# Kernel tuning notes

Measured on AMD Instinct MI355X. Metric: run time of the kernel, lower is better.

Reference implementation:

```python
import jax, jax.numpy as jnp
import numpy as np
import math

N = 100000      # num vertices
M = 50000       # num hyperedges
NNZ = 800000    # incidence entries
F_IN = 128
NHID = 128
NCLS = 40
DEPTH = 4
ALPHA = 0.1     # restart_alpha
LAMDA = 0.5


def setup_inputs() -> dict:
    key = jax.random.key(0)
    ks = jax.random.split(key, 8)
    x = jax.random.normal(ks[0], (N, F_IN), jnp.float32)
    vertex = jax.random.randint(ks[1], (NNZ,), 0, N)
    edges = jax.random.randint(ks[2], (NNZ,), 0, M)
    s0 = 1.0 / np.sqrt(F_IN)
    sh = 1.0 / np.sqrt(NHID)
    W0 = jax.random.uniform(ks[3], (F_IN, NHID), jnp.float32, -s0, s0)
    b0 = jax.random.uniform(ks[4], (NHID,), jnp.float32, -s0, s0)
    Ws = jax.random.uniform(ks[5], (DEPTH, NHID, NHID), jnp.float32, -sh, sh)
    Wout = jax.random.uniform(ks[6], (NHID, NCLS), jnp.float32, -sh, sh)
    bout = jax.random.uniform(ks[7], (NCLS,), jnp.float32, -sh, sh)
    return {"x": x, "W0": W0, "b0": b0, "Ws": Ws, "Wout": Wout,
            "bout": bout, "vertex": vertex, "edges": edges}


def reference(x, W0, b0, Ws, Wout, bout, vertex, edges):
    ones = jnp.ones((NNZ, 1), x.dtype)
    cnt_e = jnp.maximum(jax.ops.segment_sum(ones, edges, num_segments=M), 1.0)
    cnt_v = jnp.maximum(jax.ops.segment_sum(ones, vertex, num_segments=N), 1.0)

    x = jax.nn.relu(x @ W0 + b0)
    x0 = x
    for i in range(DEPTH):
        beta = math.log(LAMDA / (i + 1) + 1.0)
        # vertex -> edge mean aggregation
        Xve = x[vertex]                                          # [NNZ, NHID]
        Xe = jax.ops.segment_sum(Xve, edges, num_segments=M) / cnt_e
        # edge -> vertex mean aggregation
        Xev = Xe[edges]                                          # [NNZ, NHID]
        Xv = jax.ops.segment_sum(Xev, vertex, num_segments=N) / cnt_v
        # L2 row-normalize with detached scale (use_norm=True)
        norm = jnp.linalg.norm(Xv, axis=1, keepdims=True)
        scale = jax.lax.stop_gradient(jnp.where(norm > 0, 1.0 / norm, 0.0))
        Xv = Xv * scale
        # alpha/beta residual blend (UniGCNII)
        Xi = (1.0 - ALPHA) * Xv + ALPHA * x0
        x = jax.nn.relu((1.0 - beta) * Xi + beta * (Xi @ Ws[i]))
    return x @ Wout + bout
```

## Files before the change

kernel.cpp:

```cpp
#include <hip/hip_runtime.h>

#define NV 100000
#define NE 50000
#define NNZ_C 800000
#define CAP_E 64
#define CAP_V 48

typedef unsigned int uint32;
typedef unsigned short u16;
typedef u16 u16x8 __attribute__((ext_vector_type(8)));
typedef short short8 __attribute__((ext_vector_type(8)));
typedef float floatx4 __attribute__((ext_vector_type(4)));

__device__ __forceinline__ float bf2f(u16 h) {
  return __uint_as_float(((uint32)h) << 16);
}
__device__ __forceinline__ u16 f2bf(float f) {
  uint32 u = __float_as_uint(f);
  u += 0x7FFF + ((u >> 16) & 1);
  return (u16)(u >> 16);
}


__global__ void zero_cursors(int4* p, int n4) {
  int stride = gridDim.x * blockDim.x;
  for (int i = blockIdx.x * blockDim.x + threadIdx.x; i < n4; i += stride)
    p[i] = make_int4(0, 0, 0, 0);
}

__global__ void fill_kernel(const int* __restrict__ vertex, const int* __restrict__ edges,
                            int* __restrict__ cntE, int* __restrict__ cntV,
                            int* __restrict__ itemsE, int* __restrict__ itemsV) {
  int stride = gridDim.x * blockDim.x;
  for (int k = blockIdx.x * blockDim.x + threadIdx.x; k < NNZ_C; k += stride) {
    int e = edges[k], v = vertex[k];
    int pe = atomicAdd(&cntE[e << 4], 1);
    if (pe < CAP_E) itemsE[e * CAP_E + pe] = v;
    int pv = atomicAdd(&cntV[v << 4], 1);
    if (pv < CAP_V) itemsV[v * CAP_V + pv] = e;
  }
}


__global__ void prep_weights(const float* __restrict__ W0, const float* __restrict__ Ws,
                             u16* __restrict__ WT) {
  int idx = blockIdx.x * blockDim.x + threadIdx.x;
  if (idx >= 5 * 16384) return;
  const float betas[4] = {0.4054651081f, 0.2231435513f, 0.1541506798f, 0.1177830357f};
  int sec = idx >> 14;
  int rc = idx & 16383;
  int n = rc >> 7, k = rc & 127;
  float v;
  if (sec == 0) {
    v = W0[k * 128 + n];
  } else {
    int i = sec - 1;
    float b = betas[i];
    v = b * Ws[i * 16384 + k * 128 + n];
    if (k == n) v += 1.0f - b;
  }
  WT[idx] = f2bf(v);
}

__global__ void convert_x(const float* __restrict__ x, u16* __restrict__ xh) {
  int idx = blockIdx.x * blockDim.x + threadIdx.x;
  const float4* p = (const float4*)(x + (size_t)idx * 8);
  float4 a = p[0], b = p[1];
  u16x8 o;
  o[0] = f2bf(a.x); o[1] = f2bf(a.y); o[2] = f2bf(a.z); o[3] = f2bf(a.w);
  o[4] = f2bf(b.x); o[5] = f2bf(b.y); o[6] = f2bf(b.z); o[7] = f2bf(b.w);
  *(u16x8*)(xh + (size_t)idx * 8) = o;
}


__global__ __launch_bounds__(256) void edge_agg(const u16* __restrict__ Xh,
                                                const int* __restrict__ cntE,
                                                const int* __restrict__ itemsE,
                                                u16* __restrict__ Xeh) {
  int g = threadIdx.x >> 4;
  int lane = threadIdx.x & 15;
  int e = blockIdx.x * 16 + g;
  int cnt = cntE[e << 4];
  int n = min(cnt, CAP_E);
  const int* it = itemsE + e * CAP_E;
  float acc[8] = {0.f, 0.f, 0.f, 0.f, 0.f, 0.f, 0.f, 0.f};
  int j = 0;
  for (; j + 4 <= n; j += 4) {
    int4 vs = *(const int4*)(it + j);
    u16x8 a = *(const u16x8*)(Xh + (size_t)vs.x * 128 + lane * 8);
    u16x8 b = *(const u16x8*)(Xh + (size_t)vs.y * 128 + lane * 8);
    u16x8 c = *(const u16x8*)(Xh + (size_t)vs.z * 128 + lane * 8);
    u16x8 d = *(const u16x8*)(Xh + (size_t)vs.w * 128 + lane * 8);
    #pragma unroll
    for (int q = 0; q < 8; q++)
      acc[q] += (bf2f(a[q]) + bf2f(b[q])) + (bf2f(c[q]) + bf2f(d[q]));
  }
  for (; j < n; j++) {
    int v = it[j];
    u16x8 xv = *(const u16x8*)(Xh + (size_t)v * 128 + lane * 8);
    #pragma unroll
    for (int q = 0; q < 8; q++) acc[q] += bf2f(xv[q]);
  }
  float inv = 1.f / fmaxf((float)cnt, 1.f);
  u16x8 o;
  #pragma unroll
  for (int q = 0; q < 8; q++) o[q] = f2bf(acc[q] * inv);
  *(u16x8*)(Xeh + (size_t)e * 128 + lane * 8) = o;
}

__global__ __launch_bounds__(256) void vertex_agg(const u16* __restrict__ Xeh,
                                                  const int* __restrict__ cntV,
                                                  const int* __restrict__ itemsV,
                                                  const u16* __restrict__ x0h,
                                                  u16* __restrict__ Xih) {
  int g = threadIdx.x >> 4;
  int lane = threadIdx.x & 15;
  int v = blockIdx.x * 16 + g;
  int cnt = cntV[v << 4];
  int n = min(cnt, CAP_V);
  const int* it = itemsV + v * CAP_V;
  float acc[8] = {0.f, 0.f, 0.f, 0.f, 0.f, 0.f, 0.f, 0.f};
  int j = 0;
  for (; j + 4 <= n; j += 4) {
    int4 es = *(const int4*)(it + j);
    u16x8 a = *(const u16x8*)(Xeh + (size_t)es.x * 128 + lane * 8);
    u16x8 b = *(const u16x8*)(Xeh + (size_t)es.y * 128 + lane * 8);
    u16x8 c = *(const u16x8*)(Xeh + (size_t)es.z * 128 + lane * 8);
    u16x8 d = *(const u16x8*)(Xeh + (size_t)es.w * 128 + lane * 8);
    #pragma unroll
    for (int q = 0; q < 8; q++)
      acc[q] += (bf2f(a[q]) + bf2f(b[q])) + (bf2f(c[q]) + bf2f(d[q]));
  }
  for (; j < n; j++) {
    int e = it[j];
    u16x8 xv = *(const u16x8*)(Xeh + (size_t)e * 128 + lane * 8);
    #pragma unroll
    for (int q = 0; q < 8; q++) acc[q] += bf2f(xv[q]);
  }
  float inv = 1.f / fmaxf((float)cnt, 1.f);
  float sq = 0.f;
  #pragma unroll
  for (int q = 0; q < 8; q++) { acc[q] *= inv; sq += acc[q] * acc[q]; }
  sq += __shfl_xor(sq, 1, 64);
  sq += __shfl_xor(sq, 2, 64);
  sq += __shfl_xor(sq, 4, 64);
  sq += __shfl_xor(sq, 8, 64);
  float scale = (sq > 0.f) ? rsqrtf(sq) : 0.f;
  u16x8 x0v = *(const u16x8*)(x0h + (size_t)v * 128 + lane * 8);
  u16x8 o;
  #pragma unroll
  for (int q = 0; q < 8; q++)
    o[q] = f2bf(0.9f * acc[q] * scale + 0.1f * bf2f(x0v[q]));
  *(u16x8*)(Xih + (size_t)v * 128 + lane * 8) = o;
}


__global__ __launch_bounds__(256) void gemm_mfma(const u16* __restrict__ Ah,
                                                 const u16* __restrict__ WT,
                                                 const float* __restrict__ bias,
                                                 u16* __restrict__ Yh,
                                                 u16* __restrict__ Y2h, int nrows) {
  __shared__ u16 As[128 * 136];
  __shared__ u16 Bs[128 * 136];
  int t = threadIdx.x;
  int row0 = blockIdx.x * 128;
  #pragma unroll
  for (int i = 0; i < 8; i++) {
    int idx = t + 256 * i;
    int r = idx >> 4, c8 = idx & 15;
    u16x8 v = {0, 0, 0, 0, 0, 0, 0, 0};
    if (row0 + r < nrows) v = *(const u16x8*)(Ah + (size_t)(row0 + r) * 128 + c8 * 8);
    *(u16x8*)&As[r * 136 + c8 * 8] = v;
    u16x8 wv = *(const u16x8*)(WT + (size_t)r * 128 + c8 * 8);
    *(u16x8*)&Bs[r * 136 + c8 * 8] = wv;
  }
  __syncthreads();

  int w = t >> 6;
  int lane = t & 63;
  int lo16 = lane & 15, hi = lane >> 4;
  floatx4 acc[2][8];
  #pragma unroll
  for (int rt = 0; rt < 2; rt++)
    #pragma unroll
    for (int ct = 0; ct < 8; ct++) acc[rt][ct] = (floatx4){0.f, 0.f, 0.f, 0.f};

  #pragma unroll
  for (int kc = 0; kc < 4; kc++) {
    int koff = kc * 32 + hi * 8;
    short8 a0 = *(const short8*)&As[(w * 32 + lo16) * 136 + koff];
    short8 a1 = *(const short8*)&As[(w * 32 + 16 + lo16) * 136 + koff];
    #pragma unroll
    for (int ct = 0; ct < 8; ct++) {
      short8 b = *(const short8*)&Bs[(ct * 16 + lo16) * 136 + koff];
      acc[0][ct] = __builtin_amdgcn_mfma_f32_16x16x32_bf16(a0, b, acc[0][ct], 0, 0, 0);
      acc[1][ct] = __builtin_amdgcn_mfma_f32_16x16x32_bf16(a1, b, acc[1][ct], 0, 0, 0);
    }
  }
  __syncthreads();

  #pragma unroll
  for (int rt = 0; rt < 2; rt++) {
    #pragma unroll
    for (int ct = 0; ct < 8; ct++) {
      int col = ct * 16 + lo16;
      float bv = bias ? bias[col] : 0.f;
      #pragma unroll
      for (int reg = 0; reg < 4; reg++) {
        int row = w * 32 + rt * 16 + hi * 4 + reg;
        float v = acc[rt][ct][reg] + bv;
        v = fmaxf(v, 0.f);
        As[row * 136 + col] = f2bf(v);
      }
    }
  }
  __syncthreads();
  #pragma unroll
  for (int i = 0; i < 8; i++) {
    int idx = t + 256 * i;
    int r = idx >> 4, c8 = idx & 15;
    if (row0 + r < nrows) {
      u16x8 v = *(const u16x8*)&As[r * 136 + c8 * 8];
      *(u16x8*)(Yh + (size_t)(row0 + r) * 128 + c8 * 8) = v;
      if (Y2h) *(u16x8*)(Y2h + (size_t)(row0 + r) * 128 + c8 * 8) = v;
    }
  }
}


__global__ __launch_bounds__(256) void gemm_out(const u16* __restrict__ Xh,
                                                const float* __restrict__ W,
                                                const float* __restrict__ bias,
                                                float* __restrict__ Y, int nrows) {
  __shared__ float xs[128][36];
  __shared__ float ws[32][44];
  int t = threadIdx.x;
  int tr = t >> 3;
  int tc = t & 7;
  int row0 = blockIdx.x * 128;
  float acc[4][5];
  #pragma unroll
  for (int i = 0; i < 4; i++)
    #pragma unroll
    for (int j = 0; j < 5; j++) acc[i][j] = 0.f;

  for (int k0 = 0; k0 < 128; k0 += 32) {
    #pragma unroll
    for (int i = 0; i < 2; i++) {
      int idx = t + 256 * i;
      int r = idx >> 2, c8 = idx & 3;
      int gr = row0 + r;
      u16x8 v = {0, 0, 0, 0, 0, 0, 0, 0};
      if (gr < nrows) v = *(const u16x8*)(Xh + (size_t)gr * 128 + k0 + c8 * 8);
      #pragma unroll
      for (int q = 0; q < 8; q++) xs[r][c8 * 8 + q] = bf2f(v[q]);
    }
    #pragma unroll
    for (int i = 0; i < 5; i++) {
      int idx = t + 256 * i;
      int r = idx / 40, c = idx % 40;
      ws[r][c] = W[(k0 + r) * 40 + c];
    }
    __syncthreads();
    #pragma unroll
    for (int kk4 = 0; kk4 < 8; kk4++) {
      float4 xv[4];
      #pragma unroll
      for (int i = 0; i < 4; i++) xv[i] = *(const float4*)&xs[tr + 32 * i][kk4 * 4];
      #pragma unroll
      for (int q = 0; q < 4; q++) {
        int kk = kk4 * 4 + q;
        float w[5];
        #pragma unroll
        for (int j = 0; j < 5; j++) w[j] = ws[kk][tc * 5 + j];
        #pragma unroll
        for (int i = 0; i < 4; i++) {
          float xq = ((const float*)&xv[i])[q];
          #pragma unroll
          for (int j = 0; j < 5; j++) acc[i][j] += xq * w[j];
        }
      }
    }
    __syncthreads();
  }
  #pragma unroll
  for (int i = 0; i < 4; i++) {
    int gr = row0 + tr + 32 * i;
    if (gr >= nrows) continue;
    #pragma unroll
    for (int j = 0; j < 5; j++) {
      int c = tc * 5 + j;
      Y[(long)gr * 40 + c] = acc[i][j] + bias[c];
    }
  }
}


extern "C" void kernel_launch(void* const* d_in, const int* in_sizes, int n_in,
                              void* d_out, int out_size, void* d_ws, size_t ws_size,
                              hipStream_t stream) {
  const float* x    = (const float*)d_in[0];
  const float* W0   = (const float*)d_in[1];
  const float* b0   = (const float*)d_in[2];
  const float* Ws   = (const float*)d_in[3];
  const float* Wout = (const float*)d_in[4];
  const float* bout = (const float*)d_in[5];
  const int* vertex = (const int*)d_in[6];
  const int* edges  = (const int*)d_in[7];
  float* out = (float*)d_out;

  char* base = (char*)d_ws;
  size_t o = 0;
  auto alloc = [&](size_t bytes) -> char* {
    char* r = base + o;
    o += (bytes + 255) & ~(size_t)255;
    return r;
  };
  u16* xh     = (u16*)alloc((size_t)NV * 128 * 2);
  u16* x_curh = (u16*)alloc((size_t)NV * 128 * 2);
  u16* x0h    = (u16*)alloc((size_t)NV * 128 * 2);
  u16* Xeh    = (u16*)alloc((size_t)NE * 128 * 2);
  u16* WT     = (u16*)alloc((size_t)5 * 16384 * 2);
  int* cntE   = (int*)alloc((size_t)NE * 16 * 4);
  int* cntV   = (int*)alloc((size_t)NV * 16 * 4);
  int* itemsE = (int*)alloc((size_t)NE * CAP_E * 4);
  int* itemsV = (int*)alloc((size_t)NV * CAP_V * 4);

  int n4 = (NE * 16 + NV * 16) / 4;
  zero_cursors<<<1024, 256, 0, stream>>>((int4*)cntE, n4);
  fill_kernel<<<1024, 256, 0, stream>>>(vertex, edges, cntE, cntV, itemsE, itemsV);
  prep_weights<<<(5 * 16384 + 255) / 256, 256, 0, stream>>>(W0, Ws, WT);
  convert_x<<<(NV * 128 / 8 + 255) / 256, 256, 0, stream>>>(x, xh);

  int gblocks = (NV + 127) / 128;
  gemm_mfma<<<gblocks, 256, 0, stream>>>(xh, WT, b0, x_curh, x0h, NV);

  for (int i = 0; i < 4; i++) {
    edge_agg<<<NE / 16, 256, 0, stream>>>(x_curh, cntE, itemsE, Xeh);
    vertex_agg<<<NV / 16, 256, 0, stream>>>(Xeh, cntV, itemsV, x0h, x_curh);
    gemm_mfma<<<gblocks, 256, 0, stream>>>(x_curh, WT + (size_t)(1 + i) * 16384,
                                           nullptr, x_curh, nullptr, NV);
  }
  gemm_out<<<gblocks, 256, 0, stream>>>(x_curh, Wout, bout, out, NV);
}
```

Measured before the change: 577.1 us.

## Bucket-sort incidence build, fuse vertex aggregation into GEMM, fold x conversion

Incidence-list construction now runs in two passes: a coarse scatter into 128-key buckets packed as (local key, value) words, then a per-bucket expansion that uses shared-memory atomics for the per-key cursors. This is meant to replace the global atomics on padded per-key counters. The vertex aggregation, normalization and residual blend are fused into the layer GEMM, so Xi is built straight into LDS and never round-trips through global memory. The fp32-to-bf16 conversion of x is folded into the first GEMM's load. The cost is that the fused GEMM runs only 782 blocks, each serially gathering 128 rows, which lowers the parallelism of the gather phase.

Result: slower. 701.7 us (+21.6%).

```diff
diff --git a/kernel.cpp b/kernel.cpp
--- a/kernel.cpp
+++ b/kernel.cpp
@@ -5,6 +5,10 @@
 #define NNZ_C 800000
 #define CAP_E 64
 #define CAP_V 48
+#define NB_E 391
+#define NB_V 782
+#define CAPB_E 2560
+#define CAPB_V 1408
 
 typedef unsigned int uint32;
 typedef unsigned short u16;
@@ -22,22 +26,47 @@
 }
 
 
-__global__ void zero_cursors(int4* p, int n4) {
-  int stride = gridDim.x * blockDim.x;
-  for (int i = blockIdx.x * blockDim.x + threadIdx.x; i < n4; i += stride)
-    p[i] = make_int4(0, 0, 0, 0);
-}
-
-__global__ void fill_kernel(const int* __restrict__ vertex, const int* __restrict__ edges,
-                            int* __restrict__ cntE, int* __restrict__ cntV,
-                            int* __restrict__ itemsE, int* __restrict__ itemsV) {
+__global__ void zero_bcur(int* p, int n) {
+  int i = blockIdx.x * blockDim.x + threadIdx.x;
+  if (i < n) p[i] = 0;
+}
+
+__global__ void bucket_scatter(const int* __restrict__ vertex, const int* __restrict__ edges,
+                               int* __restrict__ bcur,
+                               uint32* __restrict__ pairE, uint32* __restrict__ pairV) {
   int stride = gridDim.x * blockDim.x;
   for (int k = blockIdx.x * blockDim.x + threadIdx.x; k < NNZ_C; k += stride) {
-    int e = edges[k], v = vertex[k];
-    int pe = atomicAdd(&cntE[e << 4], 1);
-    if (pe < CAP_E) itemsE[e * CAP_E + pe] = v;
-    int pv = atomicAdd(&cntV[v << 4], 1);
-    if (pv < CAP_V) itemsV[v * CAP_V + pv] = e;
+    uint32 e = (uint32)edges[k], v = (uint32)vertex[k];
+    uint32 be = e >> 7, bv = v >> 7;
+    int pe = atomicAdd(&bcur[be << 4], 1);
+    if (pe < CAPB_E) pairE[be * CAPB_E + pe] = ((e & 127u) << 25) | v;
+    int pv = atomicAdd(&bcur[(NB_E + bv) << 4], 1);
+    if (pv < CAPB_V) pairV[bv * CAPB_V + pv] = ((v & 127u) << 25) | e;
+  }
+}
+
+__global__ __launch_bounds__(256) void expand(const uint32* __restrict__ pairs,
+                                              const int* __restrict__ bcur, int curOff,
+                                              int capb, int* __restrict__ items, int cap,
+                                              int* __restrict__ cnt, int nKeys) {
+  __shared__ int lcnt[128];
+  int b = blockIdx.x, t = threadIdx.x;
+  if (t < 128) lcnt[t] = 0;
+  __syncthreads();
+  int n = min(bcur[(curOff + b) << 4], capb);
+  const uint32* p = pairs + (size_t)b * capb;
+  for (int i = t; i < n; i += 256) {
+    uint32 w = p[i];
+    int loc = w >> 25;
+    int val = (int)(w & 0x1FFFFFFu);
+    int r = atomicAdd(&lcnt[loc], 1);
+    int key = (b << 7) + loc;
+    if (r < cap) items[(size_t)key * cap + r] = val;
+  }
+  __syncthreads();
+  if (t < 128) {
+    int key = (b << 7) + t;
+    if (key < nKeys) cnt[key] = lcnt[t];
   }
 }
 
@@ -62,16 +91,6 @@
   WT[idx] = f2bf(v);
 }
 
-__global__ void convert_x(const float* __restrict__ x, u16* __restrict__ xh) {
-  int idx = blockIdx.x * blockDim.x + threadIdx.x;
-  const float4* p = (const float4*)(x + (size_t)idx * 8);
-  float4 a = p[0], b = p[1];
-  u16x8 o;
-  o[0] = f2bf(a.x); o[1] = f2bf(a.y); o[2] = f2bf(a.z); o[3] = f2bf(a.w);
-  o[4] = f2bf(b.x); o[5] = f2bf(b.y); o[6] = f2bf(b.z); o[7] = f2bf(b.w);
-  *(u16x8*)(xh + (size_t)idx * 8) = o;
-}
-
 
 __global__ __launch_bounds__(256) void edge_agg(const u16* __restrict__ Xh,
                                                 const int* __restrict__ cntE,
@@ -80,9 +99,9 @@
   int g = threadIdx.x >> 4;
   int lane = threadIdx.x & 15;
   int e = blockIdx.x * 16 + g;
-  int cnt = cntE[e << 4];
+  int cnt = cntE[e];
   int n = min(cnt, CAP_E);
-  const int* it = itemsE + e * CAP_E;
+  const int* it = itemsE + (size_t)e * CAP_E;
   float acc[8] = {0.f, 0.f, 0.f, 0.f, 0.f, 0.f, 0.f, 0.f};
   int j = 0;
   for (; j + 4 <= n; j += 4) {
@@ -108,58 +127,13 @@
   *(u16x8*)(Xeh + (size_t)e * 128 + lane * 8) = o;
 }
 
-__global__ __launch_bounds__(256) void vertex_agg(const u16* __restrict__ Xeh,
+
+__global__ __launch_bounds__(256) void gemm_fused(const u16* __restrict__ Xeh,
                                                   const int* __restrict__ cntV,
                                                   const int* __restrict__ itemsV,
                                                   const u16* __restrict__ x0h,
-                                                  u16* __restrict__ Xih) {
-  int g = threadIdx.x >> 4;
-  int lane = threadIdx.x & 15;
-  int v = blockIdx.x * 16 + g;
-  int cnt = cntV[v << 4];
-  int n = min(cnt, CAP_V);
-  const int* it = itemsV + v * CAP_V;
-  float acc[8] = {0.f, 0.f, 0.f, 0.f, 0.f, 0.f, 0.f, 0.f};
-  int j = 0;
-  for (; j + 4 <= n; j += 4) {
-    int4 es = *(const int4*)(it + j);
-    u16x8 a = *(const u16x8*)(Xeh + (size_t)es.x * 128 + lane * 8);
-    u16x8 b = *(const u16x8*)(Xeh + (size_t)es.y * 128 + lane * 8);
-    u16x8 c = *(const u16x8*)(Xeh + (size_t)es.z * 128 + lane * 8);
-    u16x8 d = *(const u16x8*)(Xeh + (size_t)es.w * 128 + lane * 8);
-    #pragma unroll
-    for (int q = 0; q < 8; q++)
-      acc[q] += (bf2f(a[q]) + bf2f(b[q])) + (bf2f(c[q]) + bf2f(d[q]));
-  }
-  for (; j < n; j++) {
-    int e = it[j];
-    u16x8 xv = *(const u16x8*)(Xeh + (size_t)e * 128 + lane * 8);
-    #pragma unroll
-    for (int q = 0; q < 8; q++) acc[q] += bf2f(xv[q]);
-  }
-  float inv = 1.f / fmaxf((float)cnt, 1.f);
-  float sq = 0.f;
-  #pragma unroll
-  for (int q = 0; q < 8; q++) { acc[q] *= inv; sq += acc[q] * acc[q]; }
-  sq += __shfl_xor(sq, 1, 64);
-  sq += __shfl_xor(sq, 2, 64);
-  sq += __shfl_xor(sq, 4, 64);
-  sq += __shfl_xor(sq, 8, 64);
-  float scale = (sq > 0.f) ? rsqrtf(sq) : 0.f;
-  u16x8 x0v = *(const u16x8*)(x0h + (size_t)v * 128 + lane * 8);
-  u16x8 o;
-  #pragma unroll
-  for (int q = 0; q < 8; q++)
-    o[q] = f2bf(0.9f * acc[q] * scale + 0.1f * bf2f(x0v[q]));
-  *(u16x8*)(Xih + (size_t)v * 128 + lane * 8) = o;
-}
-
-
-__global__ __launch_bounds__(256) void gemm_mfma(const u16* __restrict__ Ah,
-                                                 const u16* __restrict__ WT,
-                                                 const float* __restrict__ bias,
-                                                 u16* __restrict__ Yh,
-                                                 u16* __restrict__ Y2h, int nrows) {
+                                                  const u16* __restrict__ WT,
+                                                  u16* __restrict__ Yh, int nrows) {
   __shared__ u16 As[128 * 136];
   __shared__ u16 Bs[128 * 136];
   int t = threadIdx.x;
@@ -168,11 +142,126 @@
   for (int i = 0; i < 8; i++) {
     int idx = t + 256 * i;
     int r = idx >> 4, c8 = idx & 15;
+    *(u16x8*)&Bs[r * 136 + c8 * 8] = *(const u16x8*)(WT + (size_t)r * 128 + c8 * 8);
+  }
+  int g = t >> 4, lane = t & 15;
+  for (int pass = 0; pass < 8; pass++) {
+    int r = pass * 16 + g;
+    int v = row0 + r;
+    float acc[8] = {0.f, 0.f, 0.f, 0.f, 0.f, 0.f, 0.f, 0.f};
+    int cnt = 0;
+    if (v < nrows) {
+      cnt = cntV[v];
+      int n = min(cnt, CAP_V);
+      const int* it = itemsV + (size_t)v * CAP_V;
+      int j = 0;
+      for (; j + 4 <= n; j += 4) {
+        int4 es = *(const int4*)(it + j);
+        u16x8 a = *(const u16x8*)(Xeh + (size_t)es.x * 128 + lane * 8);
+        u16x8 b = *(const u16x8*)(Xeh + (size_t)es.y * 128 + lane * 8);
+        u16x8 c = *(const u16x8*)(Xeh + (size_t)es.z * 128 + lane * 8);
+        u16x8 d = *(const u16x8*)(Xeh + (size_t)es.w * 128 + lane * 8);
+        #pragma unroll
+        for (int q = 0; q < 8; q++)
+          acc[q] += (bf2f(a[q]) + bf2f(b[q])) + (bf2f(c[q]) + bf2f(d[q]));
+      }
+      for (; j < n; j++) {
+        int e = it[j];
+        u16x8 xv = *(const u16x8*)(Xeh + (size_t)e * 128 + lane * 8);
+        #pragma unroll
+        for (int q = 0; q < 8; q++) acc[q] += bf2f(xv[q]);
+      }
+    }
+    float inv = 1.f / fmaxf((float)cnt, 1.f);
+    float sq = 0.f;
+    #pragma unroll
+    for (int q = 0; q < 8; q++) { acc[q] *= inv; sq += acc[q] * acc[q]; }
+    sq += __shfl_xor(sq, 1, 64);
+    sq += __shfl_xor(sq, 2, 64);
+    sq += __shfl_xor(sq, 4, 64);
+    sq += __shfl_xor(sq, 8, 64);
+    float scale = (sq > 0.f) ? rsqrtf(sq) : 0.f;
+    u16x8 o = {0, 0, 0, 0, 0, 0, 0, 0};
+    if (v < nrows) {
+      u16x8 x0v = *(const u16x8*)(x0h + (size_t)v * 128 + lane * 8);
+      #pragma unroll
+      for (int q = 0; q < 8; q++)
+        o[q] = f2bf(0.9f * acc[q] * scale + 0.1f * bf2f(x0v[q]));
+    }
+    *(u16x8*)&As[r * 136 + lane * 8] = o;
+  }
+  __syncthreads();
+
+  int w = t >> 6;
+  int lane64 = t & 63;
+  int lo16 = lane64 & 15, hi = lane64 >> 4;
+  floatx4 acc[2][8];
+  #pragma unroll
+  for (int rt = 0; rt < 2; rt++)
+    #pragma unroll
+    for (int ct = 0; ct < 8; ct++) acc[rt][ct] = (floatx4){0.f, 0.f, 0.f, 0.f};
+
+  #pragma unroll
+  for (int kc = 0; kc < 4; kc++) {
+    int koff = kc * 32 + hi * 8;
+    short8 a0 = *(const short8*)&As[(w * 32 + lo16) * 136 + koff];
+    short8 a1 = *(const short8*)&As[(w * 32 + 16 + lo16) * 136 + koff];
+    #pragma unroll
+    for (int ct = 0; ct < 8; ct++) {
+      short8 b = *(const short8*)&Bs[(ct * 16 + lo16) * 136 + koff];
+      acc[0][ct] = __builtin_amdgcn_mfma_f32_16x16x32_bf16(a0, b, acc[0][ct], 0, 0, 0);
+      acc[1][ct] = __builtin_amdgcn_mfma_f32_16x16x32_bf16(a1, b, acc[1][ct], 0, 0, 0);
+    }
+  }
+  __syncthreads();
+
+  #pragma unroll
+  for (int rt = 0; rt < 2; rt++) {
+    #pragma unroll
+    for (int ct = 0; ct < 8; ct++) {
+      int col = ct * 16 + lo16;
+      #pragma unroll
+      for (int reg = 0; reg < 4; reg++) {
+        int row = w * 32 + rt * 16 + hi * 4 + reg;
+        As[row * 136 + col] = f2bf(fmaxf(acc[rt][ct][reg], 0.f));
+      }
+    }
+  }
+  __syncthreads();
+  #pragma unroll
+  for (int i = 0; i < 8; i++) {
+    int idx = t + 256 * i;
+    int r = idx >> 4, c8 = idx & 15;
+    if (row0 + r < nrows)
+      *(u16x8*)(Yh + (size_t)(row0 + r) * 128 + c8 * 8) =
+          *(const u16x8*)&As[r * 136 + c8 * 8];
+  }
+}
+
+
+__global__ __launch_bounds__(256) void gemm_first(const float* __restrict__ A,
+                                                  const u16* __restrict__ WT,
+                                                  const float* __restrict__ bias,
+                                                  u16* __restrict__ Yh,
+                                                  u16* __restrict__ Y2h, int nrows) {
+  __shared__ u16 As[128 * 136];
+  __shared__ u16 Bs[128 * 136];
+  int t = threadIdx.x;
+  int row0 = blockIdx.x * 128;
+  #pragma unroll
+  for (int i = 0; i < 8; i++) {
+    int idx = t + 256 * i;
+    int r = idx >> 4, c8 = idx & 15;
     u16x8 v = {0, 0, 0, 0, 0, 0, 0, 0};
-    if (row0 + r < nrows) v = *(const u16x8*)(Ah + (size_t)(row0 + r) * 128 + c8 * 8);
+    if (row0 + r < nrows) {
+      const float* p = A + (size_t)(row0 + r) * 128 + c8 * 8;
+      float4 a = *(const float4*)p;
+      float4 b = *(const float4*)(p + 4);
+      v[0] = f2bf(a.x); v[1] = f2bf(a.y); v[2] = f2bf(a.z); v[3] = f2bf(a.w);
+      v[4] = f2bf(b.x); v[5] = f2bf(b.y); v[6] = f2bf(b.z); v[7] = f2bf(b.w);
+    }
     *(u16x8*)&As[r * 136 + c8 * 8] = v;
-    u16x8 wv = *(const u16x8*)(WT + (size_t)r * 128 + c8 * 8);
-    *(u16x8*)&Bs[r * 136 + c8 * 8] = wv;
+    *(u16x8*)&Bs[r * 136 + c8 * 8] = *(const u16x8*)(WT + (size_t)r * 128 + c8 * 8);
   }
   __syncthreads();
 
@@ -204,13 +293,11 @@
     #pragma unroll
     for (int ct = 0; ct < 8; ct++) {
       int col = ct * 16 + lo16;
-      float bv = bias ? bias[col] : 0.f;
+      float bv = bias[col];
       #pragma unroll
       for (int reg = 0; reg < 4; reg++) {
         int row = w * 32 + rt * 16 + hi * 4 + reg;
-        float v = acc[rt][ct][reg] + bv;
-        v = fmaxf(v, 0.f);
-        As[row * 136 + col] = f2bf(v);
+        As[row * 136 + col] = f2bf(fmaxf(acc[rt][ct][reg] + bv, 0.f));
       }
     }
   }
@@ -222,7 +309,7 @@
     if (row0 + r < nrows) {
       u16x8 v = *(const u16x8*)&As[r * 136 + c8 * 8];
       *(u16x8*)(Yh + (size_t)(row0 + r) * 128 + c8 * 8) = v;
-      if (Y2h) *(u16x8*)(Y2h + (size_t)(row0 + r) * 128 + c8 * 8) = v;
+      *(u16x8*)(Y2h + (size_t)(row0 + r) * 128 + c8 * 8) = v;
     }
   }
 }
@@ -316,30 +403,32 @@
     o += (bytes + 255) & ~(size_t)255;
     return r;
   };
-  u16* xh     = (u16*)alloc((size_t)NV * 128 * 2);
   u16* x_curh = (u16*)alloc((size_t)NV * 128 * 2);
   u16* x0h    = (u16*)alloc((size_t)NV * 128 * 2);
   u16* Xeh    = (u16*)alloc((size_t)NE * 128 * 2);
   u16* WT     = (u16*)alloc((size_t)5 * 16384 * 2);
-  int* cntE   = (int*)alloc((size_t)NE * 16 * 4);
-  int* cntV   = (int*)alloc((size_t)NV * 16 * 4);
+  int* cntE   = (int*)alloc((size_t)NE * 4);
+  int* cntV   = (int*)alloc((size_t)NV * 4);
   int* itemsE = (int*)alloc((size_t)NE * CAP_E * 4);
   int* itemsV = (int*)alloc((size_t)NV * CAP_V * 4);
-
-  int n4 = (NE * 16 + NV * 16) / 4;
-  zero_cursors<<<1024, 256, 0, stream>>>((int4*)cntE, n4);
-  fill_kernel<<<1024, 256, 0, stream>>>(vertex, edges, cntE, cntV, itemsE, itemsV);
+  uint32* pairE = (uint32*)alloc((size_t)NB_E * CAPB_E * 4);
+  uint32* pairV = (uint32*)alloc((size_t)NB_V * CAPB_V * 4);
+  int* bcur   = (int*)alloc((size_t)(NB_E + NB_V) * 16 * 4);
+
+  int nb = (NB_E + NB_V) * 16;
+  zero_bcur<<<(nb + 255) / 256, 256, 0, stream>>>(bcur, nb);
+  bucket_scatter<<<1024, 256, 0, stream>>>(vertex, edges, bcur, pairE, pairV);
+  expand<<<NB_E, 256, 0, stream>>>(pairE, bcur, 0, CAPB_E, itemsE, CAP_E, cntE, NE);
+  expand<<<NB_V, 256, 0, stream>>>(pairV, bcur, NB_E, CAPB_V, itemsV, CAP_V, cntV, NV);
   prep_weights<<<(5 * 16384 + 255) / 256, 256, 0, stream>>>(W0, Ws, WT);
-  convert_x<<<(NV * 128 / 8 + 255) / 256, 256, 0, stream>>>(x, xh);
 
   int gblocks = (NV + 127) / 128;
-  gemm_mfma<<<gblocks, 256, 0, stream>>>(xh, WT, b0, x_curh, x0h, NV);
+  gemm_first<<<gblocks, 256, 0, stream>>>(x, WT, b0, x_curh, x0h, NV);
 
   for (int i = 0; i < 4; i++) {
     edge_agg<<<NE / 16, 256, 0, stream>>>(x_curh, cntE, itemsE, Xeh);
-    vertex_agg<<<NV / 16, 256, 0, stream>>>(Xeh, cntV, itemsV, x0h, x_curh);
-    gemm_mfma<<<gblocks, 256, 0, stream>>>(x_curh, WT + (size_t)(1 + i) * 16384,
-                                           nullptr, x_curh, nullptr, NV);
+    gemm_fused<<<gblocks, 256, 0, stream>>>(Xeh, cntV, itemsV, x0h,
+                                            WT + (size_t)(1 + i) * 16384, x_curh, NV);
   }
   gemm_out<<<gblocks, 256, 0, stream>>>(x_curh, Wout, bout, out, NV);
 }
```
